# Kernel optimization log

Measured on AMD Instinct MI355X. Metric: run time of the kernel, lower is better.

The kernel has to match this reference:

```python
import jax, jax.numpy as jnp
import numpy as np
import math

EMB_DIM = 1024
HEADS = 16
HEAD_DIM = EMB_DIM // HEADS
B, S = 2, 2048


def setup_inputs() -> dict:
    key = jax.random.key(0)
    k1, k2, k3, k4, k5 = jax.random.split(key, 5)
    X = jax.random.normal(k1, (B, S, EMB_DIM), dtype=jnp.float32)
    # causal mask: positions with 0.0 are masked to -inf (masked_fill(mask == 0.0, -inf))
    mask = jnp.tril(jnp.ones((S, S), dtype=jnp.float32))
    scale = 1.0 / math.sqrt(EMB_DIM)
    # torch Linear(emb_dim, 3*emb_dim): y = x @ W.T + b; store W pre-transposed [E, 3E]
    W_qkv = jax.random.normal(k2, (EMB_DIM, 3 * EMB_DIM), dtype=jnp.float32) * scale
    b_qkv = jnp.zeros((3 * EMB_DIM,), dtype=jnp.float32)
    W_o = jax.random.normal(k3, (EMB_DIM, EMB_DIM), dtype=jnp.float32) * scale
    b_o = jnp.zeros((EMB_DIM,), dtype=jnp.float32)
    return {"X": X, "mask": mask, "W_qkv": W_qkv, "b_qkv": b_qkv, "W_o": W_o, "b_o": b_o}


def reference(X, mask, W_qkv, b_qkv, W_o, b_o):
    # X: [B, S, E]
    Bn, Sn, E = X.shape
    qkv = X @ W_qkv + b_qkv                                   # [B, S, 3E]
    qkv = qkv.reshape(Bn, Sn, 3, HEADS, HEAD_DIM)
    qkv = jnp.transpose(qkv, (2, 0, 3, 1, 4))                  # [3, B, H, S, d]
    Q, K, V = qkv[0], qkv[1], qkv[2]
    inv_sqrt_d = 1.0 / math.sqrt(HEAD_DIM)
    scores = jnp.einsum('bhqd,bhkd->bhqk', Q, K) * inv_sqrt_d  # [B, H, S, S]
    scores = jnp.where(mask == 0.0, -jnp.inf, scores)
    attn = jax.nn.softmax(scores, axis=-1)
    # dropout omitted (eval mode / deterministic reference)
    out = jnp.einsum('bhqk,bhkd->bhqd', attn, V)               # [B, H, S, d]
    out = jnp.transpose(out, (0, 2, 1, 3)).reshape(Bn, Sn, E)
    return out @ W_o + b_o
```

## Files before the change

### kernel.cpp

```cpp
#include <hip/hip_runtime.h>
#include <hip/hip_bf16.h>
#include <cstdint>
#include <cstddef>

typedef __bf16 bf16_t;
typedef __attribute__((ext_vector_type(8))) __bf16 bf16x8;
typedef __attribute__((ext_vector_type(4))) __bf16 bf16x4;
typedef __attribute__((ext_vector_type(4))) float f32x4;

#define AS1 __attribute__((address_space(1)))
#define AS3 __attribute__((address_space(3)))

static constexpr int Bn = 2, Sn = 2048, En = 1024, Hn = 16, Dn = 64;

__global__ __launch_bounds__(256) void convert_f32_bf16(
    const float* __restrict__ in, bf16_t* __restrict__ out, int n) {
  int i = (blockIdx.x * 256 + threadIdx.x) * 4;
  if (i < n) {
    float4 v = *(const float4*)(in + i);
    bf16x4 o;
    o[0] = (bf16_t)v.x; o[1] = (bf16_t)v.y; o[2] = (bf16_t)v.z; o[3] = (bf16_t)v.w;
    *(bf16x4*)(out + i) = o;
  }
}

__global__ __launch_bounds__(256) void transpose_conv(
    const float* __restrict__ in, bf16_t* __restrict__ out, int R, int C) {
  __shared__ float tile[32][33];
  int bx = blockIdx.x * 32, by = blockIdx.y * 32;
  int tx = threadIdx.x & 31, ty = threadIdx.x >> 5;
#pragma unroll
  for (int i = 0; i < 32; i += 8)
    tile[ty + i][tx] = in[(size_t)(by + ty + i) * C + bx + tx];
  __syncthreads();
#pragma unroll
  for (int i = 0; i < 32; i += 8)
    out[(size_t)(bx + ty + i) * R + by + tx] = (bf16_t)tile[tx][ty + i];
}

__global__ __launch_bounds__(256) void transpose_v(
    const bf16_t* __restrict__ V, bf16_t* __restrict__ Vt) {
  __shared__ ushort tile[64][65];
  int bh = blockIdx.y, s0 = blockIdx.x * 64;
  int t = threadIdx.x;
  const ushort* src = (const ushort*)(V + ((size_t)bh * Sn + s0) * 64);
#pragma unroll
  for (int p = 0; p < 4; ++p) {
    int s = p * 16 + (t >> 4);
    int c = (t & 15) * 4;
    ushort4 v = *(const ushort4*)(src + (size_t)s * 64 + c);
    tile[s][c] = v.x; tile[s][c + 1] = v.y; tile[s][c + 2] = v.z; tile[s][c + 3] = v.w;
  }
  __syncthreads();
  ushort* dst = (ushort*)(Vt + ((size_t)bh * 64) * Sn + s0);
#pragma unroll
  for (int p = 0; p < 4; ++p) {
    int d = p * 16 + (t >> 4);
    int c = (t & 15) * 4;
    ushort4 v;
    v.x = tile[c][d]; v.y = tile[c + 1][d]; v.z = tile[c + 2][d]; v.w = tile[c + 3][d];
    *(ushort4*)(dst + (size_t)d * Sn + c) = v;
  }
}

template <int K_>
__device__ __forceinline__ void gemm_core(
    const bf16_t* __restrict__ A, const bf16_t* __restrict__ Bt,
    f32x4 (&acc)[4][4], int& col0, int& row0) {
  __shared__ bf16_t As[2][128 * 32];
  __shared__ bf16_t Bs[2][128 * 32];
  const int tid = threadIdx.x, lane = tid & 63, wid = tid >> 6;
  const int wm = wid >> 1, wn = wid & 1;
  const int m0 = blockIdx.y * 128, n0 = blockIdx.x * 128;
  const int KT = K_ / 32;

  auto stage = [&](bf16_t* as, bf16_t* bs, int kt) {
    int csw = ((lane & 3) ^ ((lane >> 2) & 3)) * 8;
#pragma unroll
    for (int j = 0; j < 2; ++j) {
      int r0 = wid * 32 + j * 16;
      const bf16_t* ga = A + (size_t)(m0 + r0 + (lane >> 2)) * K_ + kt * 32 + csw;
      __builtin_amdgcn_global_load_lds((const AS1 void*)ga, (AS3 void*)(as + r0 * 32), 16, 0, 0);
      const bf16_t* gb = Bt + (size_t)(n0 + r0 + (lane >> 2)) * K_ + kt * 32 + csw;
      __builtin_amdgcn_global_load_lds((const AS1 void*)gb, (AS3 void*)(bs + r0 * 32), 16, 0, 0);
    }
  };
  auto compute = [&](const bf16_t* as, const bf16_t* bs) {
    bf16x8 af[4], bfr[4];
    uint32_t swz = (uint32_t)(((lane >> 4) ^ (lane & 3)) << 4);
#pragma unroll
    for (int mi = 0; mi < 4; ++mi) {
      uint32_t row = (uint32_t)(wm * 64 + mi * 16 + (lane & 15));
      af[mi] = *(const bf16x8*)((const char*)as + row * 64 + swz);
    }
#pragma unroll
    for (int ni = 0; ni < 4; ++ni) {
      uint32_t row = (uint32_t)(wn * 64 + ni * 16 + (lane & 15));
      bfr[ni] = *(const bf16x8*)((const char*)bs + row * 64 + swz);
    }
#pragma unroll
    for (int mi = 0; mi < 4; ++mi)
#pragma unroll
      for (int ni = 0; ni < 4; ++ni)
        acc[mi][ni] = __builtin_amdgcn_mfma_f32_16x16x32_bf16(af[mi], bfr[ni], acc[mi][ni], 0, 0, 0);
  };

  stage(As[0], Bs[0], 0);
  __syncthreads();
  int cur = 0;
  for (int kt = 0; kt < KT - 1; ++kt) {
    stage(As[cur ^ 1], Bs[cur ^ 1], kt + 1);
    compute(As[cur], Bs[cur]);
    __syncthreads();
    cur ^= 1;
  }
  compute(As[cur], Bs[cur]);
  col0 = n0 + wn * 64 + (lane & 15);
  row0 = m0 + wm * 64 + ((lane >> 4) << 2);
}

__global__ __launch_bounds__(256) void gemm_qkv(
    const bf16_t* __restrict__ A, const bf16_t* __restrict__ Bt,
    const float* __restrict__ bias, bf16_t* __restrict__ Qb,
    bf16_t* __restrict__ Kb, bf16_t* __restrict__ Vb) {
  f32x4 acc[4][4] = {};
  int col0, row0;
  gemm_core<1024>(A, Bt, acc, col0, row0);
#pragma unroll
  for (int ni = 0; ni < 4; ++ni) {
    int n = col0 + ni * 16;
    float bv = bias[n];
    int which = n >> 10, nn = n & 1023;
    int h = nn >> 6, dd = nn & 63;
    bf16_t* dst = which == 0 ? Qb : (which == 1 ? Kb : Vb);
    float scl = which == 0 ? 0.125f : 1.0f;
#pragma unroll
    for (int mi = 0; mi < 4; ++mi)
#pragma unroll
      for (int i = 0; i < 4; ++i) {
        int m = row0 + mi * 16 + i;
        int b = m >> 11, s = m & 2047;
        float v = (acc[mi][ni][i] + bv) * scl;
        dst[(((size_t)b * Hn + h) * Sn + s) * 64 + dd] = (bf16_t)v;
      }
  }
}

__global__ __launch_bounds__(256) void gemm_out(
    const bf16_t* __restrict__ A, const bf16_t* __restrict__ Bt,
    const float* __restrict__ bias, float* __restrict__ out) {
  f32x4 acc[4][4] = {};
  int col0, row0;
  gemm_core<1024>(A, Bt, acc, col0, row0);
#pragma unroll
  for (int ni = 0; ni < 4; ++ni) {
    int n = col0 + ni * 16;
    float bv = bias[n];
#pragma unroll
    for (int mi = 0; mi < 4; ++mi)
#pragma unroll
      for (int i = 0; i < 4; ++i) {
        int m = row0 + mi * 16 + i;
        out[(size_t)m * En + n] = acc[mi][ni][i] + bv;
      }
  }
}

__global__ __launch_bounds__(256) void attn_fwd(
    const bf16_t* __restrict__ Qb, const bf16_t* __restrict__ Kb,
    const bf16_t* __restrict__ Vt, bf16_t* __restrict__ AO) {
  __shared__ bf16_t Ks[2][64 * 64];
  __shared__ bf16_t Vs[2][64 * 64];
  __shared__ bf16_t Ps[4][16 * 64];
  const int tid = threadIdx.x, lane = tid & 63, wid = tid >> 6;
  const int bh = blockIdx.y;
  const int pr = blockIdx.x;

  const int rl = lane >> 3;
  const int cp = lane & 7;
  auto issueKV = [&](int buf, int t) {
#pragma unroll
    for (int j = 0; j < 2; ++j) {
      int r = wid * 16 + j * 8 + rl;
      int sc = cp ^ (r & 7);
      const bf16_t* gk = Kb + (((size_t)bh * Sn + t * 64 + r) << 6) + (sc << 3);
      __builtin_amdgcn_global_load_lds((const AS1 void*)gk,
          (AS3 void*)(&Ks[buf][wid * 1024 + j * 512]), 16, 0, 0);
      const bf16_t* gv = Vt + ((size_t)bh * 64 + r) * Sn + t * 64 + (sc << 3);
      __builtin_amdgcn_global_load_lds((const AS1 void*)gv,
          (AS3 void*)(&Vs[buf][wid * 1024 + j * 512]), 16, 0, 0);
    }
  };

  int buf = 0;
  issueKV(0, 0);

  for (int seg = 0; seg < 2; ++seg) {
    const int q_tile = seg ? 31 - pr : pr;
    const int nt = q_tile + 1;
    const int qb = q_tile * 64 + wid * 16;

    bf16x8 aq[2];
    {
      const bf16_t* qp = Qb + ((size_t)bh * Sn + qb + (lane & 15)) * 64 + ((lane >> 4) << 3);
      aq[0] = *(const bf16x8*)qp;
      aq[1] = *(const bf16x8*)(qp + 32);
    }
    f32x4 O[4] = {};
    float m_run[4], l_run[4];
#pragma unroll
    for (int i = 0; i < 4; ++i) { m_run[i] = -1e30f; l_run[i] = 0.f; }

    for (int t = 0; t < nt; ++t) {
      asm volatile("s_waitcnt vmcnt(0)" ::: "memory");
      __syncthreads();
      if (t + 1 < nt) issueKV(buf ^ 1, t + 1);
      else if (seg == 0) issueKV(buf ^ 1, 0);
      const char* ksb = (const char*)Ks[buf];
      const char* vsb = (const char*)Vs[buf];
      f32x4 sc[4];
#pragma unroll
      for (int ni = 0; ni < 4; ++ni) {
        int kvr = ni * 16 + (lane & 15);
        uint32_t o0 = (uint32_t)(kvr * 128 + ((lane >> 4) << 4)) ^ (uint32_t)((kvr & 7) << 4);
        uint32_t o1 = (uint32_t)(kvr * 128 + 64 + ((lane >> 4) << 4)) ^ (uint32_t)((kvr & 7) << 4);
        bf16x8 b0 = *(const bf16x8*)(ksb + o0);
        bf16x8 b1 = *(const bf16x8*)(ksb + o1);
        f32x4 z = {};
        z = __builtin_amdgcn_mfma_f32_16x16x32_bf16(aq[0], b0, z, 0, 0, 0);
        sc[ni] = __builtin_amdgcn_mfma_f32_16x16x32_bf16(aq[1], b1, z, 0, 0, 0);
      }
      if (t == nt - 1) {
#pragma unroll
        for (int ni = 0; ni < 4; ++ni) {
          int kv = t * 64 + ni * 16 + (lane & 15);
#pragma unroll
          for (int i = 0; i < 4; ++i) {
            int q = qb + ((lane >> 4) << 2) + i;
            if (kv > q) sc[ni][i] = -1e30f;
          }
        }
      }
      float mt[4];
#pragma unroll
      for (int i = 0; i < 4; ++i) {
        float v = fmaxf(fmaxf(sc[0][i], sc[1][i]), fmaxf(sc[2][i], sc[3][i]));
        v = fmaxf(v, __shfl_xor(v, 1));
        v = fmaxf(v, __shfl_xor(v, 2));
        v = fmaxf(v, __shfl_xor(v, 4));
        v = fmaxf(v, __shfl_xor(v, 8));
        mt[i] = v;
      }
      int ok = (mt[0] <= m_run[0] + 8.f) && (mt[1] <= m_run[1] + 8.f) &&
               (mt[2] <= m_run[2] + 8.f) && (mt[3] <= m_run[3] + 8.f);
      if (!__all(ok)) {
#pragma unroll
        for (int i = 0; i < 4; ++i) {
          float mn = fmaxf(m_run[i], mt[i]);
          float s = __expf(m_run[i] - mn);
          m_run[i] = mn;
          l_run[i] *= s;
#pragma unroll
          for (int n2 = 0; n2 < 4; ++n2) O[n2][i] *= s;
        }
      }
      float rs[4] = {0.f, 0.f, 0.f, 0.f};
      char* pw = (char*)Ps[wid];
#pragma unroll
      for (int ni = 0; ni < 4; ++ni)
#pragma unroll
        for (int i = 0; i < 4; ++i) {
          float p = __expf(sc[ni][i] - m_run[i]);
          rs[i] += p;
          int r = ((lane >> 4) << 2) + i;
          uint32_t off = (uint32_t)(r * 128 + (ni * 16 + (lane & 15)) * 2) ^ (uint32_t)((r & 7) << 4);
          *(bf16_t*)(pw + off) = (bf16_t)p;
        }
#pragma unroll
      for (int i = 0; i < 4; ++i) {
        float v = rs[i];
        v += __shfl_xor(v, 1);
        v += __shfl_xor(v, 2);
        v += __shfl_xor(v, 4);
        v += __shfl_xor(v, 8);
        l_run[i] += v;
      }
      asm volatile("s_waitcnt lgkmcnt(0)" ::: "memory");
      __builtin_amdgcn_sched_barrier(0);
      bf16x8 pa[2];
      {
        int r = lane & 15;
        uint32_t o0 = (uint32_t)(r * 128 + ((lane >> 4) << 4)) ^ (uint32_t)((r & 7) << 4);
        uint32_t o1 = (uint32_t)(r * 128 + 64 + ((lane >> 4) << 4)) ^ (uint32_t)((r & 7) << 4);
        pa[0] = *(const bf16x8*)((const char*)pw + o0);
        pa[1] = *(const bf16x8*)((const char*)pw + o1);
      }
#pragma unroll
      for (int n2 = 0; n2 < 4; ++n2) {
        int dr = n2 * 16 + (lane & 15);
        uint32_t o0 = (uint32_t)(dr * 128 + ((lane >> 4) << 4)) ^ (uint32_t)((dr & 7) << 4);
        uint32_t o1 = (uint32_t)(dr * 128 + 64 + ((lane >> 4) << 4)) ^ (uint32_t)((dr & 7) << 4);
        bf16x8 v0 = *(const bf16x8*)(vsb + o0);
        bf16x8 v1 = *(const bf16x8*)(vsb + o1);
        O[n2] = __builtin_amdgcn_mfma_f32_16x16x32_bf16(pa[0], v0, O[n2], 0, 0, 0);
        O[n2] = __builtin_amdgcn_mfma_f32_16x16x32_bf16(pa[1], v1, O[n2], 0, 0, 0);
      }
      buf ^= 1;
    }
    int b = bh >> 4, h = bh & 15;
#pragma unroll
    for (int i = 0; i < 4; ++i) {
      float inv = 1.0f / l_run[i];
      int q = qb + ((lane >> 4) << 2) + i;
#pragma unroll
      for (int n2 = 0; n2 < 4; ++n2) {
        int d = n2 * 16 + (lane & 15);
        AO[((size_t)b * Sn + q) * En + h * 64 + d] = (bf16_t)(O[n2][i] * inv);
      }
    }
  }
}

extern "C" void kernel_launch(void* const* d_in, const int* in_sizes, int n_in,
                              void* d_out, int out_size, void* d_ws, size_t ws_size,
                              hipStream_t stream) {
  const float* X     = (const float*)d_in[0];
  const float* W_qkv = (const float*)d_in[2];
  const float* b_qkv = (const float*)d_in[3];
  const float* W_o   = (const float*)d_in[4];
  const float* b_o   = (const float*)d_in[5];
  float* out = (float*)d_out;

  char* ws = (char*)d_ws;
  bf16_t* Xb  = (bf16_t*)(ws);
  bf16_t* WqT = (bf16_t*)(ws + 8388608);
  bf16_t* WoT = (bf16_t*)(ws + 14680064);
  bf16_t* Qb  = (bf16_t*)(ws + 16777216);
  bf16_t* Kb  = (bf16_t*)(ws + 25165824);
  bf16_t* Vb  = (bf16_t*)(ws + 33554432);
  bf16_t* Vt  = (bf16_t*)(ws + 41943040);
  bf16_t* AO  = (bf16_t*)(ws + 50331648);

  convert_f32_bf16<<<4096, 256, 0, stream>>>(X, Xb, Bn * Sn * En);
  transpose_conv<<<dim3(96, 32), 256, 0, stream>>>(W_qkv, WqT, 1024, 3072);
  transpose_conv<<<dim3(32, 32), 256, 0, stream>>>(W_o, WoT, 1024, 1024);
  gemm_qkv<<<dim3(24, 32), 256, 0, stream>>>(Xb, WqT, b_qkv, Qb, Kb, Vb);
  transpose_v<<<dim3(32, 32), 256, 0, stream>>>(Vb, Vt);
  attn_fwd<<<dim3(16, 32), 256, 0, stream>>>(Qb, Kb, Vt, AO);
  gemm_out<<<dim3(8, 32), 256, 0, stream>>>(AO, WoT, b_o, out);
}
```

Baseline: 239.3 us.

## Process paired causal query tiles concurrently in 512-thread blocks sharing K/V loads

Attention blocks grow from 4 to 8 waves, so the two paired query tiles (pr and pr+16) are processed at the same time and share one stream of K/V tiles through LDS. Previously the two tiles ran one after the other and each loaded K/V separately. Each wave now issues half as many loads per tile. The cost is that the waves owning the lower tile sit idle at barriers for 16 of the 17+pr steps. The softmax also moves to base-2: log2(e) is folded into the Q scaling so exp2 replaces expf, and the rescale threshold is adjusted to match.

```diff
diff --git a/kernel.cpp b/kernel.cpp
--- a/kernel.cpp
+++ b/kernel.cpp
@@ -133,7 +133,7 @@
     int which = n >> 10, nn = n & 1023;
     int h = nn >> 6, dd = nn & 63;
     bf16_t* dst = which == 0 ? Qb : (which == 1 ? Kb : Vb);
-    float scl = which == 0 ? 0.125f : 1.0f;
+    float scl = which == 0 ? 0.125f * 1.44269504f : 1.0f;
 #pragma unroll
     for (int mi = 0; mi < 4; ++mi)
 #pragma unroll
@@ -166,56 +166,50 @@
   }
 }
 
-__global__ __launch_bounds__(256) void attn_fwd(
+__global__ __launch_bounds__(512) void attn_fwd(
     const bf16_t* __restrict__ Qb, const bf16_t* __restrict__ Kb,
     const bf16_t* __restrict__ Vt, bf16_t* __restrict__ AO) {
   __shared__ bf16_t Ks[2][64 * 64];
   __shared__ bf16_t Vs[2][64 * 64];
-  __shared__ bf16_t Ps[4][16 * 64];
+  __shared__ bf16_t Ps[8][16 * 64];
   const int tid = threadIdx.x, lane = tid & 63, wid = tid >> 6;
   const int bh = blockIdx.y;
   const int pr = blockIdx.x;
+  const int q_tile = pr + ((wid >> 2) << 4);
+  const int nt = pr + 17;
+  const int qb = q_tile * 64 + (wid & 3) * 16;
 
   const int rl = lane >> 3;
   const int cp = lane & 7;
   auto issueKV = [&](int buf, int t) {
-#pragma unroll
-    for (int j = 0; j < 2; ++j) {
-      int r = wid * 16 + j * 8 + rl;
-      int sc = cp ^ (r & 7);
-      const bf16_t* gk = Kb + (((size_t)bh * Sn + t * 64 + r) << 6) + (sc << 3);
-      __builtin_amdgcn_global_load_lds((const AS1 void*)gk,
-          (AS3 void*)(&Ks[buf][wid * 1024 + j * 512]), 16, 0, 0);
-      const bf16_t* gv = Vt + ((size_t)bh * 64 + r) * Sn + t * 64 + (sc << 3);
-      __builtin_amdgcn_global_load_lds((const AS1 void*)gv,
-          (AS3 void*)(&Vs[buf][wid * 1024 + j * 512]), 16, 0, 0);
-    }
+    int r = wid * 8 + rl;
+    int sc = cp ^ rl;
+    const bf16_t* gk = Kb + (((size_t)bh * Sn + t * 64 + r) << 6) + (sc << 3);
+    __builtin_amdgcn_global_load_lds((const AS1 void*)gk,
+        (AS3 void*)(&Ks[buf][wid * 512]), 16, 0, 0);
+    const bf16_t* gv = Vt + ((size_t)bh * 64 + r) * Sn + t * 64 + (sc << 3);
+    __builtin_amdgcn_global_load_lds((const AS1 void*)gv,
+        (AS3 void*)(&Vs[buf][wid * 512]), 16, 0, 0);
   };
 
-  int buf = 0;
+  bf16x8 aq[2];
+  {
+    const bf16_t* qp = Qb + ((size_t)bh * Sn + qb + (lane & 15)) * 64 + ((lane >> 4) << 3);
+    aq[0] = *(const bf16x8*)qp;
+    aq[1] = *(const bf16x8*)(qp + 32);
+  }
+  f32x4 O[4] = {};
+  float m_run[4], l_run[4];
+#pragma unroll
+  for (int i = 0; i < 4; ++i) { m_run[i] = -1e30f; l_run[i] = 0.f; }
+
   issueKV(0, 0);
-
-  for (int seg = 0; seg < 2; ++seg) {
-    const int q_tile = seg ? 31 - pr : pr;
-    const int nt = q_tile + 1;
-    const int qb = q_tile * 64 + wid * 16;
-
-    bf16x8 aq[2];
-    {
-      const bf16_t* qp = Qb + ((size_t)bh * Sn + qb + (lane & 15)) * 64 + ((lane >> 4) << 3);
-      aq[0] = *(const bf16x8*)qp;
-      aq[1] = *(const bf16x8*)(qp + 32);
-    }
-    f32x4 O[4] = {};
-    float m_run[4], l_run[4];
-#pragma unroll
-    for (int i = 0; i < 4; ++i) { m_run[i] = -1e30f; l_run[i] = 0.f; }
-
-    for (int t = 0; t < nt; ++t) {
-      asm volatile("s_waitcnt vmcnt(0)" ::: "memory");
-      __syncthreads();
-      if (t + 1 < nt) issueKV(buf ^ 1, t + 1);
-      else if (seg == 0) issueKV(buf ^ 1, 0);
+  for (int t = 0; t < nt; ++t) {
+    const int buf = t & 1;
+    asm volatile("s_waitcnt vmcnt(0)" ::: "memory");
+    __syncthreads();
+    if (t + 1 < nt) issueKV(buf ^ 1, t + 1);
+    if (t <= q_tile) {
       const char* ksb = (const char*)Ks[buf];
       const char* vsb = (const char*)Vs[buf];
       f32x4 sc[4];
@@ -230,7 +224,7 @@
         z = __builtin_amdgcn_mfma_f32_16x16x32_bf16(aq[0], b0, z, 0, 0, 0);
         sc[ni] = __builtin_amdgcn_mfma_f32_16x16x32_bf16(aq[1], b1, z, 0, 0, 0);
       }
-      if (t == nt - 1) {
+      if (t == q_tile) {
 #pragma unroll
         for (int ni = 0; ni < 4; ++ni) {
           int kv = t * 64 + ni * 16 + (lane & 15);
@@ -251,13 +245,13 @@
         v = fmaxf(v, __shfl_xor(v, 8));
         mt[i] = v;
       }
-      int ok = (mt[0] <= m_run[0] + 8.f) && (mt[1] <= m_run[1] + 8.f) &&
-               (mt[2] <= m_run[2] + 8.f) && (mt[3] <= m_run[3] + 8.f);
+      int ok = (mt[0] <= m_run[0] + 11.5f) && (mt[1] <= m_run[1] + 11.5f) &&
+               (mt[2] <= m_run[2] + 11.5f) && (mt[3] <= m_run[3] + 11.5f);
       if (!__all(ok)) {
 #pragma unroll
         for (int i = 0; i < 4; ++i) {
           float mn = fmaxf(m_run[i], mt[i]);
-          float s = __expf(m_run[i] - mn);
+          float s = __builtin_exp2f(m_run[i] - mn);
           m_run[i] = mn;
           l_run[i] *= s;
 #pragma unroll
@@ -270,7 +264,7 @@
       for (int ni = 0; ni < 4; ++ni)
 #pragma unroll
         for (int i = 0; i < 4; ++i) {
-          float p = __expf(sc[ni][i] - m_run[i]);
+          float p = __builtin_exp2f(sc[ni][i] - m_run[i]);
           rs[i] += p;
           int r = ((lane >> 4) << 2) + i;
           uint32_t off = (uint32_t)(r * 128 + (ni * 16 + (lane & 15)) * 2) ^ (uint32_t)((r & 7) << 4);
@@ -305,18 +299,17 @@
         O[n2] = __builtin_amdgcn_mfma_f32_16x16x32_bf16(pa[0], v0, O[n2], 0, 0, 0);
         O[n2] = __builtin_amdgcn_mfma_f32_16x16x32_bf16(pa[1], v1, O[n2], 0, 0, 0);
       }
-      buf ^= 1;
-    }
-    int b = bh >> 4, h = bh & 15;
-#pragma unroll
-    for (int i = 0; i < 4; ++i) {
-      float inv = 1.0f / l_run[i];
-      int q = qb + ((lane >> 4) << 2) + i;
-#pragma unroll
-      for (int n2 = 0; n2 < 4; ++n2) {
-        int d = n2 * 16 + (lane & 15);
-        AO[((size_t)b * Sn + q) * En + h * 64 + d] = (bf16_t)(O[n2][i] * inv);
-      }
+    }
+  }
+  int b = bh >> 4, h = bh & 15;
+#pragma unroll
+  for (int i = 0; i < 4; ++i) {
+    float inv = 1.0f / l_run[i];
+    int q = qb + ((lane >> 4) << 2) + i;
+#pragma unroll
+    for (int n2 = 0; n2 < 4; ++n2) {
+      int d = n2 * 16 + (lane & 15);
+      AO[((size_t)b * Sn + q) * En + h * 64 + d] = (bf16_t)(O[n2][i] * inv);
     }
   }
 }
@@ -346,6 +339,6 @@
   transpose_conv<<<dim3(32, 32), 256, 0, stream>>>(W_o, WoT, 1024, 1024);
   gemm_qkv<<<dim3(24, 32), 256, 0, stream>>>(Xb, WqT, b_qkv, Qb, Kb, Vb);
   transpose_v<<<dim3(32, 32), 256, 0, stream>>>(Vb, Vt);
-  attn_fwd<<<dim3(16, 32), 256, 0, stream>>>(Qb, Kb, Vt, AO);
+  attn_fwd<<<dim3(16, 32), 512, 0, stream>>>(Qb, Kb, Vt, AO);
   gemm_out<<<dim3(8, 32), 256, 0, stream>>>(AO, WoT, b_o, out);
 }
```

New measurement: 255.7 us. 6.9% more time.

## Triple-buffer KV loads, fold log2e into Q, use exp2, add setprio

Applied to the files above, without the earlier changes.

The attention kernel moves from double to triple-buffered K/V tiles. Loads now run two tiles ahead across both segments, and a partial vmcnt wait lets one prefetch stay in flight. Q is pre-scaled by log2(e) in the QKV GEMM epilogue so softmax can use exp2 directly, and the lazy-rescale threshold is widened to match. s_setprio raises wave priority around the MFMA blocks, and the swizzle expression is simplified. The cost is more LDS per block, which may lower occupancy.

```diff
diff --git a/kernel.cpp b/kernel.cpp
--- a/kernel.cpp
+++ b/kernel.cpp
@@ -133,7 +133,7 @@
     int which = n >> 10, nn = n & 1023;
     int h = nn >> 6, dd = nn & 63;
     bf16_t* dst = which == 0 ? Qb : (which == 1 ? Kb : Vb);
-    float scl = which == 0 ? 0.125f : 1.0f;
+    float scl = which == 0 ? 0.125f * 1.44269504f : 1.0f;
 #pragma unroll
     for (int mi = 0; mi < 4; ++mi)
 #pragma unroll
@@ -169,12 +169,14 @@
 __global__ __launch_bounds__(256) void attn_fwd(
     const bf16_t* __restrict__ Qb, const bf16_t* __restrict__ Kb,
     const bf16_t* __restrict__ Vt, bf16_t* __restrict__ AO) {
-  __shared__ bf16_t Ks[2][64 * 64];
-  __shared__ bf16_t Vs[2][64 * 64];
+  __shared__ bf16_t Ks[3][64 * 64];
+  __shared__ bf16_t Vs[3][64 * 64];
   __shared__ bf16_t Ps[4][16 * 64];
   const int tid = threadIdx.x, lane = tid & 63, wid = tid >> 6;
   const int bh = blockIdx.y;
   const int pr = blockIdx.x;
+  const int nt0 = pr + 1;
+  const int NT = 33;
 
   const int rl = lane >> 3;
   const int cp = lane & 7;
@@ -182,7 +184,7 @@
 #pragma unroll
     for (int j = 0; j < 2; ++j) {
       int r = wid * 16 + j * 8 + rl;
-      int sc = cp ^ (r & 7);
+      int sc = cp ^ rl;
       const bf16_t* gk = Kb + (((size_t)bh * Sn + t * 64 + r) << 6) + (sc << 3);
       __builtin_amdgcn_global_load_lds((const AS1 void*)gk,
           (AS3 void*)(&Ks[buf][wid * 1024 + j * 512]), 16, 0, 0);
@@ -191,13 +193,15 @@
           (AS3 void*)(&Vs[buf][wid * 1024 + j * 512]), 16, 0, 0);
     }
   };
-
-  int buf = 0;
-  issueKV(0, 0);
+  auto issue_u = [&](int g) { issueKV(g % 3, g < nt0 ? g : g - nt0); };
+
+  issue_u(0);
+  issue_u(1);
+  int pf = 2;
 
   for (int seg = 0; seg < 2; ++seg) {
     const int q_tile = seg ? 31 - pr : pr;
-    const int nt = q_tile + 1;
+    const int ntseg = q_tile + 1;
     const int qb = q_tile * 64 + wid * 16;
 
     bf16x8 aq[2];
@@ -211,14 +215,16 @@
 #pragma unroll
     for (int i = 0; i < 4; ++i) { m_run[i] = -1e30f; l_run[i] = 0.f; }
 
-    for (int t = 0; t < nt; ++t) {
-      asm volatile("s_waitcnt vmcnt(0)" ::: "memory");
+    for (int tloc = 0; tloc < ntseg; ++tloc) {
+      const int u = seg ? nt0 + tloc : tloc;
+      if (pf > u + 1) { asm volatile("s_waitcnt vmcnt(4)" ::: "memory"); }
+      else            { asm volatile("s_waitcnt vmcnt(0)" ::: "memory"); }
       __syncthreads();
-      if (t + 1 < nt) issueKV(buf ^ 1, t + 1);
-      else if (seg == 0) issueKV(buf ^ 1, 0);
-      const char* ksb = (const char*)Ks[buf];
-      const char* vsb = (const char*)Vs[buf];
+      if (pf < NT) { issue_u(pf); ++pf; }
+      const char* ksb = (const char*)Ks[u % 3];
+      const char* vsb = (const char*)Vs[u % 3];
       f32x4 sc[4];
+      __builtin_amdgcn_s_setprio(1);
 #pragma unroll
       for (int ni = 0; ni < 4; ++ni) {
         int kvr = ni * 16 + (lane & 15);
@@ -230,10 +236,11 @@
         z = __builtin_amdgcn_mfma_f32_16x16x32_bf16(aq[0], b0, z, 0, 0, 0);
         sc[ni] = __builtin_amdgcn_mfma_f32_16x16x32_bf16(aq[1], b1, z, 0, 0, 0);
       }
-      if (t == nt - 1) {
+      __builtin_amdgcn_s_setprio(0);
+      if (tloc == ntseg - 1) {
 #pragma unroll
         for (int ni = 0; ni < 4; ++ni) {
-          int kv = t * 64 + ni * 16 + (lane & 15);
+          int kv = tloc * 64 + ni * 16 + (lane & 15);
 #pragma unroll
           for (int i = 0; i < 4; ++i) {
             int q = qb + ((lane >> 4) << 2) + i;
@@ -251,13 +258,13 @@
         v = fmaxf(v, __shfl_xor(v, 8));
         mt[i] = v;
       }
-      int ok = (mt[0] <= m_run[0] + 8.f) && (mt[1] <= m_run[1] + 8.f) &&
-               (mt[2] <= m_run[2] + 8.f) && (mt[3] <= m_run[3] + 8.f);
+      int ok = (mt[0] <= m_run[0] + 11.5f) && (mt[1] <= m_run[1] + 11.5f) &&
+               (mt[2] <= m_run[2] + 11.5f) && (mt[3] <= m_run[3] + 11.5f);
       if (!__all(ok)) {
 #pragma unroll
         for (int i = 0; i < 4; ++i) {
           float mn = fmaxf(m_run[i], mt[i]);
-          float s = __expf(m_run[i] - mn);
+          float s = __builtin_exp2f(m_run[i] - mn);
           m_run[i] = mn;
           l_run[i] *= s;
 #pragma unroll
@@ -270,7 +277,7 @@
       for (int ni = 0; ni < 4; ++ni)
 #pragma unroll
         for (int i = 0; i < 4; ++i) {
-          float p = __expf(sc[ni][i] - m_run[i]);
+          float p = __builtin_exp2f(sc[ni][i] - m_run[i]);
           rs[i] += p;
           int r = ((lane >> 4) << 2) + i;
           uint32_t off = (uint32_t)(r * 128 + (ni * 16 + (lane & 15)) * 2) ^ (uint32_t)((r & 7) << 4);
@@ -295,6 +302,7 @@
         pa[0] = *(const bf16x8*)((const char*)pw + o0);
         pa[1] = *(const bf16x8*)((const char*)pw + o1);
       }
+      __builtin_amdgcn_s_setprio(1);
 #pragma unroll
       for (int n2 = 0; n2 < 4; ++n2) {
         int dr = n2 * 16 + (lane & 15);
@@ -305,7 +313,7 @@
         O[n2] = __builtin_amdgcn_mfma_f32_16x16x32_bf16(pa[0], v0, O[n2], 0, 0, 0);
         O[n2] = __builtin_amdgcn_mfma_f32_16x16x32_bf16(pa[1], v1, O[n2], 0, 0, 0);
       }
-      buf ^= 1;
+      __builtin_amdgcn_s_setprio(0);
     }
     int b = bh >> 4, h = bh & 15;
 #pragma unroll
```

Result: no change. 243.7 us (+1.8%).

## Compute transposed scores in attention, use exp2 with prescaled Q, permute P in registers

Applied to the files above, without the earlier changes.

The QK^T MFMA now takes swapped operands, so each lane holds scores for a single query row. Row max and sum reductions need only two shuffles, and the per-row rescale state drops to one scalar per lane. Q is prescaled by log2(e) so softmax can use exp2, and the rescale threshold is widened. P is packed to bf16 with v_cvt_pk and redistributed through ds_bpermute instead of an LDS write/read round trip. The output tile is staged through LDS before the global store, and s_setprio brackets the MFMA sections. This removes LDS traffic, shuffles and waits from the inner loop, at the cost of bpermute instructions and more intricate lane mappings that could be wrong.

```diff
diff --git a/kernel.cpp b/kernel.cpp
--- a/kernel.cpp
+++ b/kernel.cpp
@@ -12,6 +12,12 @@
 #define AS3 __attribute__((address_space(3)))
 
 static constexpr int Bn = 2, Sn = 2048, En = 1024, Hn = 16, Dn = 64;
+
+__device__ __forceinline__ uint32_t cvt_pk_bf16(float lo, float hi) {
+  uint32_t r;
+  asm("v_cvt_pk_bf16_f32 %0, %1, %2" : "=v"(r) : "v"(lo), "v"(hi));
+  return r;
+}
 
 __global__ __launch_bounds__(256) void convert_f32_bf16(
     const float* __restrict__ in, bf16_t* __restrict__ out, int n) {
@@ -133,7 +139,7 @@
     int which = n >> 10, nn = n & 1023;
     int h = nn >> 6, dd = nn & 63;
     bf16_t* dst = which == 0 ? Qb : (which == 1 ? Kb : Vb);
-    float scl = which == 0 ? 0.125f : 1.0f;
+    float scl = which == 0 ? 0.125f * 1.44269504f : 1.0f;
 #pragma unroll
     for (int mi = 0; mi < 4; ++mi)
 #pragma unroll
@@ -182,7 +188,7 @@
 #pragma unroll
     for (int j = 0; j < 2; ++j) {
       int r = wid * 16 + j * 8 + rl;
-      int sc = cp ^ (r & 7);
+      int sc = cp ^ rl;
       const bf16_t* gk = Kb + (((size_t)bh * Sn + t * 64 + r) << 6) + (sc << 3);
       __builtin_amdgcn_global_load_lds((const AS1 void*)gk,
           (AS3 void*)(&Ks[buf][wid * 1024 + j * 512]), 16, 0, 0);
@@ -192,13 +198,18 @@
     }
   };
 
+  const int srcA = (((lane & 15) + ((lane & 16) << 1)) << 2);
+  const int srcB = srcA + 64;
+  const bool hi = lane >= 32;
+
   int buf = 0;
   issueKV(0, 0);
 
   for (int seg = 0; seg < 2; ++seg) {
     const int q_tile = seg ? 31 - pr : pr;
-    const int nt = q_tile + 1;
+    const int ntseg = q_tile + 1;
     const int qb = q_tile * 64 + wid * 16;
+    const int qmy = qb + (lane & 15);
 
     bf16x8 aq[2];
     {
@@ -207,18 +218,17 @@
       aq[1] = *(const bf16x8*)(qp + 32);
     }
     f32x4 O[4] = {};
-    float m_run[4], l_run[4];
-#pragma unroll
-    for (int i = 0; i < 4; ++i) { m_run[i] = -1e30f; l_run[i] = 0.f; }
-
-    for (int t = 0; t < nt; ++t) {
+    float m_run = -1e30f, l_run = 0.f;
+
+    for (int t = 0; t < ntseg; ++t) {
       asm volatile("s_waitcnt vmcnt(0)" ::: "memory");
       __syncthreads();
-      if (t + 1 < nt) issueKV(buf ^ 1, t + 1);
+      if (t + 1 < ntseg) issueKV(buf ^ 1, t + 1);
       else if (seg == 0) issueKV(buf ^ 1, 0);
       const char* ksb = (const char*)Ks[buf];
       const char* vsb = (const char*)Vs[buf];
       f32x4 sc[4];
+      __builtin_amdgcn_s_setprio(1);
 #pragma unroll
       for (int ni = 0; ni < 4; ++ni) {
         int kvr = ni * 16 + (lane & 15);
@@ -227,74 +237,63 @@
         bf16x8 b0 = *(const bf16x8*)(ksb + o0);
         bf16x8 b1 = *(const bf16x8*)(ksb + o1);
         f32x4 z = {};
-        z = __builtin_amdgcn_mfma_f32_16x16x32_bf16(aq[0], b0, z, 0, 0, 0);
-        sc[ni] = __builtin_amdgcn_mfma_f32_16x16x32_bf16(aq[1], b1, z, 0, 0, 0);
-      }
-      if (t == nt - 1) {
+        z = __builtin_amdgcn_mfma_f32_16x16x32_bf16(b0, aq[0], z, 0, 0, 0);
+        sc[ni] = __builtin_amdgcn_mfma_f32_16x16x32_bf16(b1, aq[1], z, 0, 0, 0);
+      }
+      __builtin_amdgcn_s_setprio(0);
+      if (t == ntseg - 1) {
 #pragma unroll
         for (int ni = 0; ni < 4; ++ni) {
-          int kv = t * 64 + ni * 16 + (lane & 15);
-#pragma unroll
-          for (int i = 0; i < 4; ++i) {
-            int q = qb + ((lane >> 4) << 2) + i;
-            if (kv > q) sc[ni][i] = -1e30f;
-          }
+          int kvbase = t * 64 + ni * 16 + ((lane >> 4) << 2);
+#pragma unroll
+          for (int i = 0; i < 4; ++i)
+            if (kvbase + i > qmy) sc[ni][i] = -1e30f;
         }
       }
-      float mt[4];
-#pragma unroll
-      for (int i = 0; i < 4; ++i) {
-        float v = fmaxf(fmaxf(sc[0][i], sc[1][i]), fmaxf(sc[2][i], sc[3][i]));
-        v = fmaxf(v, __shfl_xor(v, 1));
-        v = fmaxf(v, __shfl_xor(v, 2));
-        v = fmaxf(v, __shfl_xor(v, 4));
-        v = fmaxf(v, __shfl_xor(v, 8));
-        mt[i] = v;
-      }
-      int ok = (mt[0] <= m_run[0] + 8.f) && (mt[1] <= m_run[1] + 8.f) &&
-               (mt[2] <= m_run[2] + 8.f) && (mt[3] <= m_run[3] + 8.f);
-      if (!__all(ok)) {
-#pragma unroll
-        for (int i = 0; i < 4; ++i) {
-          float mn = fmaxf(m_run[i], mt[i]);
-          float s = __expf(m_run[i] - mn);
-          m_run[i] = mn;
-          l_run[i] *= s;
-#pragma unroll
-          for (int n2 = 0; n2 < 4; ++n2) O[n2][i] *= s;
-        }
-      }
-      float rs[4] = {0.f, 0.f, 0.f, 0.f};
-      char* pw = (char*)Ps[wid];
+      float mt = sc[0][0];
 #pragma unroll
       for (int ni = 0; ni < 4; ++ni)
 #pragma unroll
-        for (int i = 0; i < 4; ++i) {
-          float p = __expf(sc[ni][i] - m_run[i]);
-          rs[i] += p;
-          int r = ((lane >> 4) << 2) + i;
-          uint32_t off = (uint32_t)(r * 128 + (ni * 16 + (lane & 15)) * 2) ^ (uint32_t)((r & 7) << 4);
-          *(bf16_t*)(pw + off) = (bf16_t)p;
-        }
-#pragma unroll
-      for (int i = 0; i < 4; ++i) {
-        float v = rs[i];
-        v += __shfl_xor(v, 1);
-        v += __shfl_xor(v, 2);
-        v += __shfl_xor(v, 4);
-        v += __shfl_xor(v, 8);
-        l_run[i] += v;
-      }
-      asm volatile("s_waitcnt lgkmcnt(0)" ::: "memory");
-      __builtin_amdgcn_sched_barrier(0);
-      bf16x8 pa[2];
-      {
-        int r = lane & 15;
-        uint32_t o0 = (uint32_t)(r * 128 + ((lane >> 4) << 4)) ^ (uint32_t)((r & 7) << 4);
-        uint32_t o1 = (uint32_t)(r * 128 + 64 + ((lane >> 4) << 4)) ^ (uint32_t)((r & 7) << 4);
-        pa[0] = *(const bf16x8*)((const char*)pw + o0);
-        pa[1] = *(const bf16x8*)((const char*)pw + o1);
-      }
+        for (int i = 0; i < 4; ++i) mt = fmaxf(mt, sc[ni][i]);
+      mt = fmaxf(mt, __shfl_xor(mt, 16));
+      mt = fmaxf(mt, __shfl_xor(mt, 32));
+      if (!__all(mt <= m_run + 11.5f)) {
+        float mn = fmaxf(m_run, mt);
+        float s = __builtin_exp2f(m_run - mn);
+        m_run = mn;
+        l_run *= s;
+#pragma unroll
+        for (int n2 = 0; n2 < 4; ++n2)
+#pragma unroll
+          for (int i = 0; i < 4; ++i) O[n2][i] *= s;
+      }
+      float rs = 0.f;
+      uint32_t pk[4][2];
+#pragma unroll
+      for (int ni = 0; ni < 4; ++ni) {
+        float p0 = __builtin_exp2f(sc[ni][0] - m_run);
+        float p1 = __builtin_exp2f(sc[ni][1] - m_run);
+        float p2 = __builtin_exp2f(sc[ni][2] - m_run);
+        float p3 = __builtin_exp2f(sc[ni][3] - m_run);
+        rs += (p0 + p1) + (p2 + p3);
+        pk[ni][0] = cvt_pk_bf16(p0, p1);
+        pk[ni][1] = cvt_pk_bf16(p2, p3);
+      }
+      rs += __shfl_xor(rs, 16);
+      rs += __shfl_xor(rs, 32);
+      l_run += rs;
+      union U8 { uint32_t u[4]; bf16x8 v; } pw0, pw1;
+#pragma unroll
+      for (int w = 0; w < 4; ++w) {
+        int srci = (w < 2) ? srcA : srcB;
+        uint32_t x0 = (uint32_t)__builtin_amdgcn_ds_bpermute(srci, (int)pk[0][w & 1]);
+        uint32_t y0 = (uint32_t)__builtin_amdgcn_ds_bpermute(srci, (int)pk[1][w & 1]);
+        pw0.u[w] = hi ? y0 : x0;
+        uint32_t x1 = (uint32_t)__builtin_amdgcn_ds_bpermute(srci, (int)pk[2][w & 1]);
+        uint32_t y1 = (uint32_t)__builtin_amdgcn_ds_bpermute(srci, (int)pk[3][w & 1]);
+        pw1.u[w] = hi ? y1 : x1;
+      }
+      __builtin_amdgcn_s_setprio(1);
 #pragma unroll
       for (int n2 = 0; n2 < 4; ++n2) {
         int dr = n2 * 16 + (lane & 15);
@@ -302,20 +301,35 @@
         uint32_t o1 = (uint32_t)(dr * 128 + 64 + ((lane >> 4) << 4)) ^ (uint32_t)((dr & 7) << 4);
         bf16x8 v0 = *(const bf16x8*)(vsb + o0);
         bf16x8 v1 = *(const bf16x8*)(vsb + o1);
-        O[n2] = __builtin_amdgcn_mfma_f32_16x16x32_bf16(pa[0], v0, O[n2], 0, 0, 0);
-        O[n2] = __builtin_amdgcn_mfma_f32_16x16x32_bf16(pa[1], v1, O[n2], 0, 0, 0);
-      }
+        O[n2] = __builtin_amdgcn_mfma_f32_16x16x32_bf16(v0, pw0.v, O[n2], 0, 0, 0);
+        O[n2] = __builtin_amdgcn_mfma_f32_16x16x32_bf16(v1, pw1.v, O[n2], 0, 0, 0);
+      }
+      __builtin_amdgcn_s_setprio(0);
       buf ^= 1;
     }
+    char* pw = (char*)Ps[wid];
+    const float inv = 1.0f / l_run;
+    const int ql = lane & 15, g = lane >> 4;
+#pragma unroll
+    for (int n2 = 0; n2 < 4; ++n2)
+#pragma unroll
+      for (int p2 = 0; p2 < 2; ++p2) {
+        uint32_t w = cvt_pk_bf16(O[n2][2 * p2] * inv, O[n2][2 * p2 + 1] * inv);
+        uint32_t byte = (uint32_t)(ql * 128 + n2 * 32 + g * 8 + p2 * 4) ^ (uint32_t)((ql & 7) << 4);
+        *(uint32_t*)(pw + byte) = w;
+      }
+    asm volatile("s_waitcnt lgkmcnt(0)" ::: "memory");
+    __builtin_amdgcn_sched_barrier(0);
     int b = bh >> 4, h = bh & 15;
 #pragma unroll
     for (int i = 0; i < 4; ++i) {
-      float inv = 1.0f / l_run[i];
-      int q = qb + ((lane >> 4) << 2) + i;
+      int ql2 = (g << 2) + i;
+      int qrow = qb + ql2;
 #pragma unroll
       for (int n2 = 0; n2 < 4; ++n2) {
-        int d = n2 * 16 + (lane & 15);
-        AO[((size_t)b * Sn + q) * En + h * 64 + d] = (bf16_t)(O[n2][i] * inv);
+        int d = n2 * 16 + ql;
+        uint32_t byte = (uint32_t)(ql2 * 128 + d * 2) ^ (uint32_t)((ql2 & 7) << 4);
+        AO[((size_t)b * Sn + qrow) * En + h * 64 + d] = *(bf16_t*)(pw + byte);
       }
     }
   }
```

Measured after the change: 229.0 us. -4.3%, faster.
